# Performance work log

Hardware: AMD Instinct MI355X
Metric: run time of the kernel (lower is better)

Reference implementation:

```python
import jax, jax.numpy as jnp
import numpy as np

LOG_2PI = float(np.log(2.0 * np.pi))


def setup_inputs() -> dict:
    key = jax.random.key(0)
    k1, k2, k3 = jax.random.split(key, 3)
    N, D, K = 2_000_000, 16, 32
    data = jax.random.normal(k1, (N, D), dtype=jnp.float32)
    means = jax.random.uniform(k2, (K, D), dtype=jnp.float32)  # torch.rand init
    # torch init is eye expanded per component; perturb slightly so the
    # Cholesky / solve paths are exercised with non-trivial values while
    # A @ A.T stays well-conditioned PD.
    cov_parts = (jnp.eye(D, dtype=jnp.float32)[None, :, :]
                 + 0.1 * jax.random.normal(k3, (K, D, D), dtype=jnp.float32))
    log_weights = jnp.zeros((K,), dtype=jnp.float32)
    return {"data": data, "means": means, "cov_parts": cov_parts,
            "log_weights": log_weights}


def _mixture_loglik(data, means, cov_parts, log_weights):
    D = data.shape[-1]
    # covariance_k = A_k @ A_k^T  -> Cholesky factor L_k (lower)
    cov = jnp.einsum('kij,klj->kil', cov_parts, cov_parts)      # [K, D, D]
    chol = jnp.linalg.cholesky(cov)                             # [K, D, D]

    def comp_logprob(mu, L):
        # MVN log_prob for one component over all N points
        diff = data - mu                                        # [N, D]
        # solve L z = diff^T  -> z: [D, N]
        z = jax.scipy.linalg.solve_triangular(L, diff.T, lower=True)
        quad = jnp.sum(z * z, axis=0)                           # [N]
        logdet = jnp.sum(jnp.log(jnp.diagonal(L)))              # 0.5*logdet(cov)
        return -0.5 * (quad + D * LOG_2PI) - logdet             # [N]

    # [N, K] log-likelihood per point per component
    log_liks = jax.vmap(comp_logprob, in_axes=(0, 0), out_axes=1)(means, chol)
    weighted = log_liks + log_weights ** 2                      # note: squared, per source
    return jnp.mean(jax.nn.logsumexp(weighted, axis=1))


def reference(data, means, cov_parts, log_weights):
    return _mixture_loglik(data, means, cov_parts, log_weights)
```

## Files before the change

### kernel.cpp

```cpp
#include <hip/hip_runtime.h>
#include <math.h>


#define LOG_2PI 1.8378770664093453f
#define INV_LN2 1.4426950408889634f
#define LN2_D   0.6931471805599453

typedef float    float4v __attribute__((ext_vector_type(4)));
typedef float    f32x16  __attribute__((ext_vector_type(16)));
typedef _Float16 f16x8   __attribute__((ext_vector_type(8)));
typedef _Float16 f16x2   __attribute__((ext_vector_type(2)));

union H8 { f16x8 h8; f16x2 h2[4]; };

#if __has_builtin(__builtin_amdgcn_exp2f)
#define EXP2F(x) __builtin_amdgcn_exp2f(x)
#else
#define EXP2F(x) exp2f(x)
#endif
#if __has_builtin(__builtin_amdgcn_logf)
#define LOG2F(x) __builtin_amdgcn_logf(x)
#else
#define LOG2F(x) log2f(x)
#endif

static __device__ __forceinline__ f16x2 pk2(float a, float b) {
#if __has_builtin(__builtin_amdgcn_cvt_pkrtz)
  return __builtin_bit_cast(f16x2, __builtin_amdgcn_cvt_pkrtz(a, b));
#else
  f16x2 r; r[0] = (_Float16)a; r[1] = (_Float16)b; return r;
#endif
}

static __device__ __forceinline__ unsigned swapd(unsigned u, bool lo) {
#if __has_builtin(__builtin_amdgcn_permlane32_swap)
  typedef unsigned u32x2 __attribute__((ext_vector_type(2)));
  u32x2 r = __builtin_amdgcn_permlane32_swap(u, u, false, false);
  return lo ? r[1] : r[0];
#else
  return (unsigned)__shfl_xor((int)u, 32, 64);
#endif
}
static __device__ __forceinline__ float partner32(float x, bool lo) {
  return __builtin_bit_cast(float, swapd(__builtin_bit_cast(unsigned, x), lo));
}
static __device__ __forceinline__ f16x2 swap2(f16x2 v, bool lo) {
  return __builtin_bit_cast(f16x2, swapd(__builtin_bit_cast(unsigned, v), lo));
}
static __device__ __forceinline__ f16x2 sel2(bool c, f16x2 a, f16x2 b) {
  unsigned ua = __builtin_bit_cast(unsigned, a);
  unsigned ub = __builtin_bit_cast(unsigned, b);
  return __builtin_bit_cast(f16x2, c ? ua : ub);
}

__global__ void setup_kernel(const float* __restrict__ means,
                             const float* __restrict__ cov_parts,
                             const float* __restrict__ log_weights,
                             _Float16* __restrict__ W)
{
  const int k = blockIdx.x;
  const int i = threadIdx.x;

  __shared__ float sA[16][17];
  __shared__ float sC[16][17];
  __shared__ float sMu[16];
  __shared__ float sR[16];

  if (i < 16) {
    #pragma unroll
    for (int j = 0; j < 16; ++j) sA[i][j] = cov_parts[(k*16 + i)*16 + j];
    sMu[i] = means[k*16 + i];
  }
  __syncthreads();

  if (i < 16) {
    #pragma unroll
    for (int j = 0; j < 16; ++j) {
      float acc = 0.f;
      #pragma unroll
      for (int l = 0; l < 16; ++l) acc += sA[i][l] * sA[j][l];
      sC[i][j] = acc;
    }
  }
  __syncthreads();

  for (int j = 0; j < 16; ++j) {
    if (i == j) {
      float d = sC[j][j];
      for (int l = 0; l < j; ++l) d -= sC[j][l]*sC[j][l];
      sC[j][j] = sqrtf(d);
    }
    __syncthreads();
    if (i < 16 && i > j) {
      float a = sC[i][j];
      for (int l = 0; l < j; ++l) a -= sC[i][l]*sC[j][l];
      sC[i][j] = a / sC[j][j];
    }
    __syncthreads();
  }

  if (i < 16) {
    float y[16];
    #pragma unroll
    for (int r = 0; r < 16; ++r) {
      float a = (r == i) ? 1.f : 0.f;
      #pragma unroll
      for (int l = 0; l < r; ++l) a -= sC[r][l] * y[l];
      y[r] = a / sC[r][r];
    }
    #pragma unroll
    for (int r = 0; r < 16; ++r) sA[r][i] = y[r];
  }
  __syncthreads();

  if (i < 16) {
    float p[16];
    #pragma unroll
    for (int j = 0; j < 16; ++j) {
      float acc = 0.f;
      #pragma unroll
      for (int l = 0; l < 16; ++l) acc += sA[l][i] * sA[l][j];
      p[j] = acc;
    }
    float ri = 0.f;
    #pragma unroll
    for (int j = 0; j < 16; ++j) ri += p[j] * sMu[j];
    sR[i] = ri;

    #pragma unroll
    for (int j = 0; j < 16; ++j) {
      W[(size_t)(i*64 + (k + 32*(j >> 3)))*8 + (j & 7)] =
          (_Float16)(-0.5f * INV_LN2 * p[j]);
    }
    W[(size_t)(16*64 + (k + 32*(i >> 3)))*8 + (i & 7)] =
        (_Float16)(INV_LN2 * ri);
  }
  __syncthreads();

  if (i == 0) {
    float logdet = 0.f;
    #pragma unroll
    for (int j = 0; j < 16; ++j) logdet += __logf(sC[j][j]);
    float mupmu = 0.f;
    #pragma unroll
    for (int j = 0; j < 16; ++j) mupmu += sMu[j] * sR[j];
    float lw = log_weights[k];
    float c2v = INV_LN2 * (-0.5f*(mupmu + 16.f*LOG_2PI) - logdet + lw*lw);
    #pragma unroll
    for (int v = 0; v < 8; ++v) {
      W[(size_t)(17*64 + k)*8 + v]      = (v == 0) ? (_Float16)c2v : (_Float16)0.f;
      W[(size_t)(17*64 + k + 32)*8 + v] = (_Float16)0.f;
    }
  }
}

__global__ __launch_bounds__(256, 2) void main_kernel(
    const float* __restrict__ data,
    const _Float16* __restrict__ W,
    float* __restrict__ partials,
    int npairs)
{
  const int lane = threadIdx.x & 63;
  const int n32  = lane & 31;
  const bool lo  = lane < 32;
  const int gwave  = (int)((blockIdx.x * blockDim.x + threadIdx.x) >> 6);
  const int nwaves = (int)((gridDim.x * blockDim.x) >> 6);

  f16x8 Wf[18];
  #pragma unroll
  for (int c = 0; c < 18; ++c)
    Wf[c] = *(const f16x8*)(W + (size_t)(c*64 + lane)*8);

  H8 bC;
  #pragma unroll
  for (int j = 0; j < 4; ++j) bC.h2[j] = pk2(0.f, 0.f);
  if (lo) bC.h2[0] = pk2(1.f, 0.f);

  float accsum = 0.f;

  const char* base = (const char*)data + ((size_t)n32*64 + (lo ? 0 : 32));
  auto paddr = [&](int p) { return base + (size_t)p*4096; };

  float4v sa0[2], sa1[2], sb0[2], sb1[2];

  {
    const char* q0 = (gwave           < npairs) ? paddr(gwave)          : base;
    const char* q1 = (gwave + nwaves  < npairs) ? paddr(gwave + nwaves) : base;
    sa0[0] = *(const float4v*)(q0);        sa1[0] = *(const float4v*)(q0 + 16);
    sb0[0] = *(const float4v*)(q0 + 2048); sb1[0] = *(const float4v*)(q0 + 2064);
    sa0[1] = *(const float4v*)(q1);        sa1[1] = *(const float4v*)(q1 + 16);
    sb0[1] = *(const float4v*)(q1 + 2048); sb1[1] = *(const float4v*)(q1 + 2064);
  }

  int p = gwave;
  while (p < npairs) {
    #pragma unroll
    for (int slot = 0; slot < 2; ++slot) {
      if (p >= npairs) break;

      f16x2 ownA[4], ownB[4];
      ownA[0] = pk2(sa0[slot][0], sa0[slot][1]);
      ownA[1] = pk2(sa0[slot][2], sa0[slot][3]);
      ownA[2] = pk2(sa1[slot][0], sa1[slot][1]);
      ownA[3] = pk2(sa1[slot][2], sa1[slot][3]);
      ownB[0] = pk2(sb0[slot][0], sb0[slot][1]);
      ownB[1] = pk2(sb0[slot][2], sb0[slot][3]);
      ownB[2] = pk2(sb1[slot][0], sb1[slot][1]);
      ownB[3] = pk2(sb1[slot][2], sb1[slot][3]);

      {
        int np_ = p + 2*nwaves;
        const char* q = (np_ < npairs) ? paddr(np_) : base;
        sa0[slot] = *(const float4v*)(q);        sa1[slot] = *(const float4v*)(q + 16);
        sb0[slot] = *(const float4v*)(q + 2048); sb1[slot] = *(const float4v*)(q + 2064);
      }

      f16x2 xhA[8], xhB[8];
      #pragma unroll
      for (int j = 0; j < 4; ++j) {
        f16x2 oA = swap2(ownA[j], lo);
        f16x2 oB = swap2(ownB[j], lo);
        xhA[j]   = sel2(lo, ownA[j], oA);
        xhA[4+j] = sel2(lo, oA, ownA[j]);
        xhB[j]   = sel2(lo, ownB[j], oB);
        xhB[4+j] = sel2(lo, oB, ownB[j]);
      }

      f32x16 accA, accB;
      #pragma unroll
      for (int r = 0; r < 16; ++r) { accA[r] = 0.f; accB[r] = 0.f; }

      #pragma unroll
      for (int c = 0; c < 16; ++c) {
        _Float16 xiA = xhA[c >> 1][c & 1];
        H8 bA;
        #pragma unroll
        for (int j = 0; j < 4; ++j) bA.h2[j] = ownA[j] * xiA;
        accA = __builtin_amdgcn_mfma_f32_32x32x16_f16(Wf[c], bA.h8, accA, 0, 0, 0);
        _Float16 xiB = xhB[c >> 1][c & 1];
        H8 bB;
        #pragma unroll
        for (int j = 0; j < 4; ++j) bB.h2[j] = ownB[j] * xiB;
        accB = __builtin_amdgcn_mfma_f32_32x32x16_f16(Wf[c], bB.h8, accB, 0, 0, 0);
      }
      {
        H8 bA, bB;
        #pragma unroll
        for (int j = 0; j < 4; ++j) { bA.h2[j] = ownA[j]; bB.h2[j] = ownB[j]; }
        accA = __builtin_amdgcn_mfma_f32_32x32x16_f16(Wf[16], bA.h8, accA, 0, 0, 0);
        accB = __builtin_amdgcn_mfma_f32_32x32x16_f16(Wf[16], bB.h8, accB, 0, 0, 0);
      }
      {
        accA = __builtin_amdgcn_mfma_f32_32x32x16_f16(Wf[17], bC.h8, accA, 0, 0, 0);
        accB = __builtin_amdgcn_mfma_f32_32x32x16_f16(Wf[17], bC.h8, accB, 0, 0, 0);
      }

      {
        float m = accA[0];
        #pragma unroll
        for (int r = 1; r < 16; ++r) m = fmaxf(m, accA[r]);
        m = fmaxf(m, partner32(m, lo));
        float s = 0.f;
        #pragma unroll
        for (int r = 0; r < 16; ++r) s += EXP2F(accA[r] - m);
        s += partner32(s, lo);
        accsum += m + LOG2F(s);
      }
      {
        float m = accB[0];
        #pragma unroll
        for (int r = 1; r < 16; ++r) m = fmaxf(m, accB[r]);
        m = fmaxf(m, partner32(m, lo));
        float s = 0.f;
        #pragma unroll
        for (int r = 0; r < 16; ++r) s += EXP2F(accB[r] - m);
        s += partner32(s, lo);
        accsum += m + LOG2F(s);
      }

      p += nwaves;
    }
  }

  #pragma unroll
  for (int off = 1; off <= 32; off <<= 1)
    accsum += __shfl_xor(accsum, off, 64);

  __shared__ float wsum[4];
  const int wid = (int)(threadIdx.x >> 6);
  if ((threadIdx.x & 63) == 0) wsum[wid] = accsum;
  __syncthreads();
  if (threadIdx.x == 0)
    partials[blockIdx.x] = wsum[0] + wsum[1] + wsum[2] + wsum[3];
}

__global__ void reduce_kernel(const float* __restrict__ partials, int n,
                              float* __restrict__ out, double scale)
{
  __shared__ double sd[256];
  double a = 0.0;
  for (int idx = threadIdx.x; idx < n; idx += 256) a += (double)partials[idx];
  sd[threadIdx.x] = a;
  __syncthreads();
  for (int s = 128; s > 0; s >>= 1) {
    if ((int)threadIdx.x < s) sd[threadIdx.x] += sd[threadIdx.x + s];
    __syncthreads();
  }
  if (threadIdx.x == 0) out[0] = (float)(sd[0] * scale);
}

extern "C" void kernel_launch(void* const* d_in, const int* in_sizes, int n_in,
                              void* d_out, int out_size, void* d_ws, size_t ws_size,
                              hipStream_t stream)
{
  const float* data        = (const float*)d_in[0];
  const float* means       = (const float*)d_in[1];
  const float* cov_parts   = (const float*)d_in[2];
  const float* log_weights = (const float*)d_in[3];

  const int npts   = in_sizes[0] / 16;
  const int npairs = npts / 64;

  _Float16* W      = (_Float16*)d_ws;
  float*    partials = (float*)((char*)d_ws + (size_t)18*64*8*sizeof(_Float16));

  const int GRID = 512, BLOCK = 256;
  setup_kernel<<<32, 64, 0, stream>>>(means, cov_parts, log_weights, W);
  main_kernel<<<GRID, BLOCK, 0, stream>>>(data, W, partials, npairs);
  reduce_kernel<<<1, 256, 0, stream>>>(partials, GRID, (float*)d_out,
                                       LN2_D / (2.0 * (double)npts));
}
```

Measured before the change: 205.5 us.

## Exploit symmetric quadratic form to halve MFMA count per point pair

The quadratic term x^T P x was previously expanded over all 16x16 products, giving 16 MFMAs plus a linear and a constant MFMA. It is now expanded over only the unique upper-triangle products, using diagonal offsets d=0..8 with off-diagonal weights doubled, and the linear and constant terms are packed into a single tenth MFMA. The setup kernel writes the matching 10-chunk weight layout. Fewer weight registers lets launch bounds rise to 3 blocks per CU with a larger grid, at the cost of more shuffle and select work to build the operands.

```diff
diff --git a/kernel.cpp b/kernel.cpp
--- a/kernel.cpp
+++ b/kernel.cpp
@@ -58,7 +58,7 @@
                              const float* __restrict__ log_weights,
                              _Float16* __restrict__ W)
 {
-  const int k = blockIdx.x;
+  const int m = blockIdx.x;
   const int i = threadIdx.x;
 
   __shared__ float sA[16][17];
@@ -68,8 +68,8 @@
 
   if (i < 16) {
     #pragma unroll
-    for (int j = 0; j < 16; ++j) sA[i][j] = cov_parts[(k*16 + i)*16 + j];
-    sMu[i] = means[k*16 + i];
+    for (int j = 0; j < 16; ++j) sA[i][j] = cov_parts[(m*16 + i)*16 + j];
+    sMu[i] = means[m*16 + i];
   }
   __syncthreads();
 
@@ -126,35 +126,28 @@
     #pragma unroll
     for (int j = 0; j < 16; ++j) ri += p[j] * sMu[j];
     sR[i] = ri;
-
-    #pragma unroll
-    for (int j = 0; j < 16; ++j) {
-      W[(size_t)(i*64 + (k + 32*(j >> 3)))*8 + (j & 7)] =
-          (_Float16)(-0.5f * INV_LN2 * p[j]);
-    }
-    W[(size_t)(16*64 + (k + 32*(i >> 3)))*8 + (i & 7)] =
-        (_Float16)(INV_LN2 * ri);
-  }
-  __syncthreads();
-
-  if (i == 0) {
-    float logdet = 0.f;
-    #pragma unroll
-    for (int j = 0; j < 16; ++j) logdet += __logf(sC[j][j]);
-    float mupmu = 0.f;
-    #pragma unroll
-    for (int j = 0; j < 16; ++j) mupmu += sMu[j] * sR[j];
-    float lw = log_weights[k];
-    float c2v = INV_LN2 * (-0.5f*(mupmu + 16.f*LOG_2PI) - logdet + lw*lw);
-    #pragma unroll
-    for (int v = 0; v < 8; ++v) {
-      W[(size_t)(17*64 + k)*8 + v]      = (v == 0) ? (_Float16)c2v : (_Float16)0.f;
-      W[(size_t)(17*64 + k + 32)*8 + v] = (_Float16)0.f;
-    }
-  }
-}
-
-__global__ __launch_bounds__(256, 2) void main_kernel(
+    __syncthreads();
+
+    const int h = i >> 3, v = i & 7;
+    const int lw_ = m + 32*h;
+    #pragma unroll
+    for (int d = 0; d < 8; ++d) {
+      float sc = (d == 0) ? -0.5f*INV_LN2 : -INV_LN2;
+      W[(size_t)(d*64 + lw_)*8 + v] = (_Float16)(sc * p[(i + d) & 15]);
+    }
+    if (h == 0) W[(size_t)(8*64 + m)*8      + v] = (_Float16)(-INV_LN2 * p[i + 8]);
+    else        W[(size_t)(8*64 + m + 32)*8 + v] = (_Float16)( INV_LN2 * sR[v]);
+    float logdet = 0.f, mupmu = 0.f;
+    #pragma unroll
+    for (int j = 0; j < 16; ++j) { logdet += __logf(sC[j][j]); mupmu += sMu[j]*sR[j]; }
+    float lwv = log_weights[m];
+    float c2v = INV_LN2 * (-0.5f*(mupmu + 16.f*LOG_2PI) - logdet + lwv*lwv);
+    if (h == 0) W[(size_t)(9*64 + m)*8      + v] = (_Float16)(INV_LN2 * sR[8 + v]);
+    else        W[(size_t)(9*64 + m + 32)*8 + v] = (v == 0) ? (_Float16)c2v : (_Float16)0.f;
+  }
+}
+
+__global__ __launch_bounds__(256, 3) void main_kernel(
     const float* __restrict__ data,
     const _Float16* __restrict__ W,
     float* __restrict__ partials,
@@ -166,15 +159,13 @@
   const int gwave  = (int)((blockIdx.x * blockDim.x + threadIdx.x) >> 6);
   const int nwaves = (int)((gridDim.x * blockDim.x) >> 6);
 
-  f16x8 Wf[18];
+  f16x8 Wf[10];
   #pragma unroll
-  for (int c = 0; c < 18; ++c)
+  for (int c = 0; c < 10; ++c)
     Wf[c] = *(const f16x8*)(W + (size_t)(c*64 + lane)*8);
 
-  H8 bC;
-  #pragma unroll
-  for (int j = 0; j < 4; ++j) bC.h2[j] = pk2(0.f, 0.f);
-  if (lo) bC.h2[0] = pk2(1.f, 0.f);
+  const f16x2 kOne  = pk2(1.f, 0.f);
+  const f16x2 kZero = pk2(0.f, 0.f);
 
   float accsum = 0.f;
 
@@ -182,10 +173,9 @@
   auto paddr = [&](int p) { return base + (size_t)p*4096; };
 
   float4v sa0[2], sa1[2], sb0[2], sb1[2];
-
   {
-    const char* q0 = (gwave           < npairs) ? paddr(gwave)          : base;
-    const char* q1 = (gwave + nwaves  < npairs) ? paddr(gwave + nwaves) : base;
+    const char* q0 = (gwave          < npairs) ? paddr(gwave)          : base;
+    const char* q1 = (gwave + nwaves < npairs) ? paddr(gwave + nwaves) : base;
     sa0[0] = *(const float4v*)(q0);        sa1[0] = *(const float4v*)(q0 + 16);
     sb0[0] = *(const float4v*)(q0 + 2048); sb1[0] = *(const float4v*)(q0 + 2064);
     sa0[1] = *(const float4v*)(q1);        sa1[1] = *(const float4v*)(q1 + 16);
@@ -198,15 +188,20 @@
     for (int slot = 0; slot < 2; ++slot) {
       if (p >= npairs) break;
 
-      f16x2 ownA[4], ownB[4];
-      ownA[0] = pk2(sa0[slot][0], sa0[slot][1]);
-      ownA[1] = pk2(sa0[slot][2], sa0[slot][3]);
-      ownA[2] = pk2(sa1[slot][0], sa1[slot][1]);
-      ownA[3] = pk2(sa1[slot][2], sa1[slot][3]);
-      ownB[0] = pk2(sb0[slot][0], sb0[slot][1]);
-      ownB[1] = pk2(sb0[slot][2], sb0[slot][3]);
-      ownB[2] = pk2(sb1[slot][0], sb1[slot][1]);
-      ownB[3] = pk2(sb1[slot][2], sb1[slot][3]);
+      f16x2 uA[8], uB[8];
+      uA[0] = pk2(sa0[slot][0], sa0[slot][1]);
+      uA[1] = pk2(sa0[slot][2], sa0[slot][3]);
+      uA[2] = pk2(sa1[slot][0], sa1[slot][1]);
+      uA[3] = pk2(sa1[slot][2], sa1[slot][3]);
+      uB[0] = pk2(sb0[slot][0], sb0[slot][1]);
+      uB[1] = pk2(sb0[slot][2], sb0[slot][3]);
+      uB[2] = pk2(sb1[slot][0], sb1[slot][1]);
+      uB[3] = pk2(sb1[slot][2], sb1[slot][3]);
+      #pragma unroll
+      for (int j = 0; j < 4; ++j) {
+        uA[4+j] = swap2(uA[j], lo);
+        uB[4+j] = swap2(uB[j], lo);
+      }
 
       {
         int np_ = p + 2*nwaves;
@@ -215,67 +210,67 @@
         sb0[slot] = *(const float4v*)(q + 2048); sb1[slot] = *(const float4v*)(q + 2064);
       }
 
-      f16x2 xhA[8], xhB[8];
-      #pragma unroll
-      for (int j = 0; j < 4; ++j) {
-        f16x2 oA = swap2(ownA[j], lo);
-        f16x2 oB = swap2(ownB[j], lo);
-        xhA[j]   = sel2(lo, ownA[j], oA);
-        xhA[4+j] = sel2(lo, oA, ownA[j]);
-        xhB[j]   = sel2(lo, ownB[j], oB);
-        xhB[4+j] = sel2(lo, oB, ownB[j]);
-      }
-
       f32x16 accA, accB;
       #pragma unroll
       for (int r = 0; r < 16; ++r) { accA[r] = 0.f; accB[r] = 0.f; }
 
       #pragma unroll
-      for (int c = 0; c < 16; ++c) {
-        _Float16 xiA = xhA[c >> 1][c & 1];
-        H8 bA;
-        #pragma unroll
-        for (int j = 0; j < 4; ++j) bA.h2[j] = ownA[j] * xiA;
-        accA = __builtin_amdgcn_mfma_f32_32x32x16_f16(Wf[c], bA.h8, accA, 0, 0, 0);
-        _Float16 xiB = xhB[c >> 1][c & 1];
-        H8 bB;
-        #pragma unroll
-        for (int j = 0; j < 4; ++j) bB.h2[j] = ownB[j] * xiB;
-        accB = __builtin_amdgcn_mfma_f32_32x32x16_f16(Wf[c], bB.h8, accB, 0, 0, 0);
+      for (int d = 0; d < 9; ++d) {
+        H8 bA, bB;
+        #pragma unroll
+        for (int j = 0; j < 4; ++j) {
+          const int o = 2*j + d;
+          f16x2 rA, rB;
+          if ((d & 1) == 0) { rA = uA[o >> 1]; rB = uB[o >> 1]; }
+          else {
+            rA = __builtin_shufflevector(uA[(o-1) >> 1], uA[(o+1) >> 1], 1, 2);
+            rB = __builtin_shufflevector(uB[(o-1) >> 1], uB[(o+1) >> 1], 1, 2);
+          }
+          f16x2 pA = uA[j] * rA;
+          f16x2 pB = uB[j] * rB;
+          if (d == 8) {
+            pA = sel2(lo, pA, uA[4+j]);
+            pB = sel2(lo, pB, uB[4+j]);
+          }
+          bA.h2[j] = pA; bB.h2[j] = pB;
+        }
+        accA = __builtin_amdgcn_mfma_f32_32x32x16_f16(Wf[d], bA.h8, accA, 0, 0, 0);
+        accB = __builtin_amdgcn_mfma_f32_32x32x16_f16(Wf[d], bB.h8, accB, 0, 0, 0);
       }
       {
         H8 bA, bB;
-        #pragma unroll
-        for (int j = 0; j < 4; ++j) { bA.h2[j] = ownA[j]; bB.h2[j] = ownB[j]; }
-        accA = __builtin_amdgcn_mfma_f32_32x32x16_f16(Wf[16], bA.h8, accA, 0, 0, 0);
-        accB = __builtin_amdgcn_mfma_f32_32x32x16_f16(Wf[16], bB.h8, accB, 0, 0, 0);
-      }
+        bA.h2[0] = sel2(lo, uA[4], kOne);
+        bB.h2[0] = sel2(lo, uB[4], kOne);
+        #pragma unroll
+        for (int j = 1; j < 4; ++j) {
+          bA.h2[j] = sel2(lo, uA[4+j], kZero);
+          bB.h2[j] = sel2(lo, uB[4+j], kZero);
+        }
+        accA = __builtin_amdgcn_mfma_f32_32x32x16_f16(Wf[9], bA.h8, accA, 0, 0, 0);
+        accB = __builtin_amdgcn_mfma_f32_32x32x16_f16(Wf[9], bB.h8, accB, 0, 0, 0);
+      }
+
       {
-        accA = __builtin_amdgcn_mfma_f32_32x32x16_f16(Wf[17], bC.h8, accA, 0, 0, 0);
-        accB = __builtin_amdgcn_mfma_f32_32x32x16_f16(Wf[17], bC.h8, accB, 0, 0, 0);
-      }
-
+        float mx = accA[0];
+        #pragma unroll
+        for (int r = 1; r < 16; ++r) mx = fmaxf(mx, accA[r]);
+        mx = fmaxf(mx, partner32(mx, lo));
+        float s = 0.f;
+        #pragma unroll
+        for (int r = 0; r < 16; ++r) s += EXP2F(accA[r] - mx);
+        s += partner32(s, lo);
+        accsum += mx + LOG2F(s);
+      }
       {
-        float m = accA[0];
-        #pragma unroll
-        for (int r = 1; r < 16; ++r) m = fmaxf(m, accA[r]);
-        m = fmaxf(m, partner32(m, lo));
+        float mx = accB[0];
+        #pragma unroll
+        for (int r = 1; r < 16; ++r) mx = fmaxf(mx, accB[r]);
+        mx = fmaxf(mx, partner32(mx, lo));
         float s = 0.f;
         #pragma unroll
-        for (int r = 0; r < 16; ++r) s += EXP2F(accA[r] - m);
+        for (int r = 0; r < 16; ++r) s += EXP2F(accB[r] - mx);
         s += partner32(s, lo);
-        accsum += m + LOG2F(s);
-      }
-      {
-        float m = accB[0];
-        #pragma unroll
-        for (int r = 1; r < 16; ++r) m = fmaxf(m, accB[r]);
-        m = fmaxf(m, partner32(m, lo));
-        float s = 0.f;
-        #pragma unroll
-        for (int r = 0; r < 16; ++r) s += EXP2F(accB[r] - m);
-        s += partner32(s, lo);
-        accsum += m + LOG2F(s);
+        accsum += mx + LOG2F(s);
       }
 
       p += nwaves;
@@ -322,9 +317,9 @@
   const int npairs = npts / 64;
 
   _Float16* W      = (_Float16*)d_ws;
-  float*    partials = (float*)((char*)d_ws + (size_t)18*64*8*sizeof(_Float16));
-
-  const int GRID = 512, BLOCK = 256;
+  float*    partials = (float*)((char*)d_ws + (size_t)10*64*8*sizeof(_Float16));
+
+  const int GRID = 768, BLOCK = 256;
   setup_kernel<<<32, 64, 0, stream>>>(means, cov_parts, log_weights, W);
   main_kernel<<<GRID, BLOCK, 0, stream>>>(data, W, partials, npairs);
   reduce_kernel<<<1, 256, 0, stream>>>(partials, GRID, (float*)d_out,
```

Measured after the change: 206.0 us. About the same (+0.2%).
